# Performance work log

Hardware: AMD Instinct MI355X
Metric: run time of the kernel (lower is better)

## Reference

```python
import jax, jax.numpy as jnp
import numpy as np

INPUT_SIZE = 1024
MEMORY_SIZE = 32768
MEMORY_DIM = 128
TOP_K = 32
EPS = 1e-8


def _linear_params(key, fan_in, fan_out):
    kw, kb = jax.random.split(key)
    bound = 1.0 / np.sqrt(fan_in)
    W = jax.random.uniform(kw, (fan_out, fan_in), jnp.float32, -bound, bound)
    b = jax.random.uniform(kb, (fan_out,), jnp.float32, -bound, bound)
    return W, b


def setup_inputs() -> dict:
    key = jax.random.key(0)
    kx, km, k1, k2, k3 = jax.random.split(key, 5)
    x = jax.random.normal(kx, (16, INPUT_SIZE), jnp.float32)
    # xavier_uniform for the memory table
    xav = np.sqrt(6.0 / (MEMORY_SIZE + MEMORY_DIM))
    memory = jax.random.uniform(km, (MEMORY_SIZE, MEMORY_DIM), jnp.float32, -xav, xav)
    Ww, bw = _linear_params(k1, INPUT_SIZE, MEMORY_DIM)   # write_proj
    Wr, br = _linear_params(k2, INPUT_SIZE, MEMORY_DIM)   # read_proj
    Wo, bo = _linear_params(k3, MEMORY_DIM, INPUT_SIZE)   # output_proj
    return {"x": x, "memory": memory, "Ww": Ww, "bw": bw,
            "Wr": Wr, "br": br, "Wo": Wo, "bo": bo}


def reference(x, memory, Ww, bw, Wr, br, Wo, bo):
    # x: [B, I]; memory: [M, D] (prev_memory=None path -> shared table per batch)
    write_vector = x @ Ww.T + bw          # [B, D]
    read_query = x @ Wr.T + br            # [B, D]

    # cosine similarity of each query against every memory slot: [B, M]
    qn = jnp.maximum(jnp.linalg.norm(read_query, axis=-1, keepdims=True), EPS)  # [B, 1]
    mn = jnp.maximum(jnp.linalg.norm(memory, axis=-1), EPS)                      # [M]
    similarity = (read_query @ memory.T) / (qn * mn[None, :])

    # top-k slots; the scatter-built one-hot bmm is just a gather + sum
    _, top_idx = jax.lax.top_k(similarity, TOP_K)        # [B, k] int32
    retrieved = memory[top_idx].sum(axis=1)              # [B, D]

    output = retrieved @ Wo.T + bo                        # [B, I]

    write_strength = jax.nn.sigmoid(
        jnp.sum(write_vector * retrieved, axis=-1, keepdims=True))  # [B, 1]
    # outer-product update [B,1,D] broadcast-added over all M slots
    update = (write_strength * write_vector)[:, None, :]  # [B, 1, D]
    new_memory = memory[None, :, :] + update              # [B, M, D]
    return output, new_memory
```

## Files before the change

### kernel.cpp

```cpp
#include <hip/hip_runtime.h>
#include <math.h>

#define BATCH 16
#define ISZ   1024
#define MSZ   32768
#define DSZ   128
#define TOPK  32
#define EPSV  1e-8f
#define NCHUNK 32
#define CHUNK  (MSZ / NCHUNK)
#define CPL    (CHUNK / 64)

__global__ void proj_kernel(const float* __restrict__ x,
                            const float* __restrict__ Ww, const float* __restrict__ bw,
                            const float* __restrict__ Wr, const float* __restrict__ br,
                            float* __restrict__ wv, float* __restrict__ rq) {
    int d = blockIdx.x;
    int b = blockIdx.y;
    int lane = threadIdx.x;
    const float* xr  = x  + (size_t)b * ISZ;
    const float* wwr = Ww + (size_t)d * ISZ;
    const float* wrr = Wr + (size_t)d * ISZ;
    float aw = 0.f, ar = 0.f;
    for (int j = lane; j < ISZ; j += 64) {
        float xv = xr[j];
        aw = fmaf(xv, wwr[j], aw);
        ar = fmaf(xv, wrr[j], ar);
    }
    for (int off = 32; off; off >>= 1) {
        aw += __shfl_down(aw, off);
        ar += __shfl_down(ar, off);
    }
    if (lane == 0) {
        wv[b * DSZ + d] = aw + bw[d];
        rq[b * DSZ + d] = ar + br[d];
    }
}

__global__ __launch_bounds__(128)
void sim_kernel(const float* __restrict__ rq,
                const float* __restrict__ memory, float* __restrict__ sim) {
    __shared__ float qn_s[BATCH];
    int tid = threadIdx.x;
    {
        int b = tid >> 3, seg = tid & 7;
        float a = 0.f;
        #pragma unroll
        for (int j = 0; j < 16; ++j) {
            float v = rq[b * DSZ + seg * 16 + j];
            a = fmaf(v, v, a);
        }
        for (int off = 4; off; off >>= 1) a += __shfl_down(a, off, 8);
        if (seg == 0) qn_s[b] = fmaxf(sqrtf(a), EPSV);
    }
    __syncthreads();

    int r = blockIdx.x * 128 + tid;
    const float4* row = (const float4*)(memory + (size_t)r * DSZ);
    const float4* rq4 = (const float4*)rq;
    float acc[BATCH];
    #pragma unroll
    for (int b = 0; b < BATCH; ++b) acc[b] = 0.f;
    float nrm = 0.f;
    #pragma unroll 4
    for (int j = 0; j < 32; ++j) {
        float4 v = row[j];
        nrm = fmaf(v.x, v.x, fmaf(v.y, v.y, fmaf(v.z, v.z, fmaf(v.w, v.w, nrm))));
        #pragma unroll
        for (int b = 0; b < BATCH; ++b) {
            float4 q = rq4[b * 32 + j];
            acc[b] = fmaf(v.x, q.x, fmaf(v.y, q.y, fmaf(v.z, q.z, fmaf(v.w, q.w, acc[b]))));
        }
    }
    float mnr = fmaxf(sqrtf(nrm), EPSV);
    #pragma unroll
    for (int b = 0; b < BATCH; ++b)
        sim[(size_t)b * MSZ + r] = acc[b] / (qn_s[b] * mnr);
}

__global__ __launch_bounds__(256)
void ptopk_kernel(const float* __restrict__ sim,
                  float* __restrict__ cand_v, int* __restrict__ cand_i) {
    int lane = threadIdx.x & 63;
    int task = blockIdx.x * 4 + (threadIdx.x >> 6);
    int b     = task >> 5;
    int chunk = task & 31;
    int base  = chunk * CHUNK;
    const float* s = sim + (size_t)b * MSZ + base;

    float val[CPL];
    #pragma unroll
    for (int i = 0; i < CPL; ++i) val[i] = s[i * 64 + lane];

    float keep_v = -INFINITY; int keep_i = 0x7FFFFFFF;
    for (int k = 0; k < TOPK; ++k) {
        float lv = -INFINITY; int li = 0x7FFFFFFF;
        #pragma unroll
        for (int i = 0; i < CPL; ++i) {
            int gi = base + i * 64 + lane;
            bool better = val[i] > lv;
            lv = better ? val[i] : lv;
            li = better ? gi : li;
        }
        float bv = lv; int bi = li;
        #pragma unroll
        for (int off = 32; off; off >>= 1) {
            float ov = __shfl_xor(bv, off);
            int   oi = __shfl_xor(bi, off);
            if (ov > bv || (ov == bv && oi < bi)) { bv = ov; bi = oi; }
        }
        if (lane == k) { keep_v = bv; keep_i = bi; }
        #pragma unroll
        for (int i = 0; i < CPL; ++i) {
            int gi = base + i * 64 + lane;
            val[i] = (gi == bi) ? -INFINITY : val[i];
        }
    }
    if (lane < TOPK) {
        cand_v[task * TOPK + lane] = keep_v;
        cand_i[task * TOPK + lane] = keep_i;
    }
}

__global__ __launch_bounds__(128)
void merge_kernel(const float* __restrict__ cand_v, const int* __restrict__ cand_i,
                  const float* __restrict__ memory, const float* __restrict__ wv,
                  const float* __restrict__ Wo, const float* __restrict__ bo,
                  float* __restrict__ out, float* __restrict__ u) {
    __shared__ int   topi[TOPK];
    __shared__ float r_s[DSZ];
    __shared__ float s_sh;
    int b = blockIdx.x;
    int tid = threadIdx.x;
    int lane = tid & 63;
    const int NC = NCHUNK * TOPK;
    const int PL = NC / 64;

    if (tid < 64) {
        float val[PL]; int idx[PL];
        #pragma unroll
        for (int i = 0; i < PL; ++i) {
            val[i] = cand_v[b * NC + i * 64 + lane];
            idx[i] = cand_i[b * NC + i * 64 + lane];
        }
        for (int k = 0; k < TOPK; ++k) {
            float lv = -INFINITY; int li = 0x7FFFFFFF;
            #pragma unroll
            for (int i = 0; i < PL; ++i) {
                bool better = (val[i] > lv) || (val[i] == lv && idx[i] < li);
                lv = better ? val[i] : lv;
                li = better ? idx[i] : li;
            }
            float bv = lv; int bi = li;
            #pragma unroll
            for (int off = 32; off; off >>= 1) {
                float ov = __shfl_xor(bv, off);
                int   oi = __shfl_xor(bi, off);
                if (ov > bv || (ov == bv && oi < bi)) { bv = ov; bi = oi; }
            }
            if (lane == k) topi[lane] = bi;
            #pragma unroll
            for (int i = 0; i < PL; ++i)
                val[i] = (idx[i] == bi) ? -INFINITY : val[i];
        }
    }
    __syncthreads();

    float rsum = 0.f;
    for (int k = 0; k < TOPK; ++k)
        rsum += memory[(size_t)topi[k] * DSZ + tid];
    r_s[tid] = rsum;
    __syncthreads();

    if (tid < 64) {
        float a = wv[b * DSZ + tid] * r_s[tid] + wv[b * DSZ + 64 + tid] * r_s[64 + tid];
        for (int off = 32; off; off >>= 1) a += __shfl_down(a, off);
        if (tid == 0) s_sh = 1.f / (1.f + expf(-a));
    }
    __syncthreads();
    u[b * DSZ + tid] = s_sh * wv[b * DSZ + tid];

    const float4* r4 = (const float4*)r_s;
    for (int i = tid; i < ISZ; i += 128) {
        const float4* w4 = (const float4*)(Wo + (size_t)i * DSZ);
        float acc = 0.f;
        #pragma unroll 8
        for (int j = 0; j < 32; ++j) {
            float4 w = w4[j];
            float4 r = r4[j];
            acc = fmaf(w.x, r.x, fmaf(w.y, r.y, fmaf(w.z, r.z, fmaf(w.w, r.w, acc))));
        }
        out[b * ISZ + i] = acc + bo[i];
    }
}

__global__ void bcast_kernel(const float* __restrict__ memory, const float* __restrict__ u,
                             float* __restrict__ out_nm) {
    __shared__ float4 u_s[BATCH * DSZ / 4];
    int tid = threadIdx.x;
    const float4* u4 = (const float4*)u;
    for (int i = tid; i < BATCH * DSZ / 4; i += 256) u_s[i] = u4[i];
    __syncthreads();
    size_t f = (size_t)blockIdx.x * 256 + tid;
    float4 m4 = ((const float4*)memory)[f];
    int d4 = (int)(f & 31);
    float4* o = (float4*)out_nm;
    #pragma unroll
    for (int b = 0; b < BATCH; ++b) {
        float4 uv = u_s[b * 32 + d4];
        float4 r = make_float4(m4.x + uv.x, m4.y + uv.y, m4.z + uv.z, m4.w + uv.w);
        o[(size_t)b * (MSZ * DSZ / 4) + f] = r;
    }
}

extern "C" void kernel_launch(void* const* d_in, const int* in_sizes, int n_in,
                              void* d_out, int out_size, void* d_ws, size_t ws_size,
                              hipStream_t stream) {
    const float* x      = (const float*)d_in[0];
    const float* memory = (const float*)d_in[1];
    const float* Ww     = (const float*)d_in[2];
    const float* bw     = (const float*)d_in[3];
    const float* Wr     = (const float*)d_in[4];
    const float* br     = (const float*)d_in[5];
    const float* Wo     = (const float*)d_in[6];
    const float* bo     = (const float*)d_in[7];

    float* out    = (float*)d_out;
    float* out_nm = out + BATCH * ISZ;

    float* ws        = (float*)d_ws;
    float* wv        = ws;
    float* rq        = wv + BATCH * DSZ;
    float* sim       = rq + BATCH * DSZ;
    float* cand_v    = sim + (size_t)BATCH * MSZ;
    int*   cand_i    = (int*)(cand_v + BATCH * NCHUNK * TOPK);
    float* u         = (float*)(cand_i + BATCH * NCHUNK * TOPK);

    proj_kernel<<<dim3(DSZ, BATCH), 64, 0, stream>>>(x, Ww, bw, Wr, br, wv, rq);
    sim_kernel<<<MSZ / 128, 128, 0, stream>>>(rq, memory, sim);
    ptopk_kernel<<<(BATCH * NCHUNK) / 4, 256, 0, stream>>>(sim, cand_v, cand_i);
    merge_kernel<<<BATCH, 128, 0, stream>>>(cand_v, cand_i, memory, wv, Wo, bo, out, u);
    bcast_kernel<<<MSZ * DSZ / 4 / 256, 256, 0, stream>>>(memory, u, out_nm);
}
```

Baseline: 173.9 us.

## Fuse all five stages into one persistent kernel with grid barriers

Replaces the five separate launches (projection, similarity, partial top-k, merge, broadcast) with a single persistent kernel of 256 blocks that separates the stages with software grid-wide barriers built on atomics. Work in each stage is remapped onto the fixed grid, and the final broadcast loops over 16 tiles per block. This targets launch overhead and inter-kernel gaps, but leaves many blocks idle in the narrow stages (merge uses only 16 blocks, top-k uses half the waves). It also needs an extra memset and relies on all 256 blocks being co-resident to avoid deadlock.

```diff
diff --git a/kernel.cpp b/kernel.cpp
--- a/kernel.cpp
+++ b/kernel.cpp
@@ -10,39 +10,76 @@
 #define NCHUNK 32
 #define CHUNK  (MSZ / NCHUNK)
 #define CPL    (CHUNK / 64)
-
-__global__ void proj_kernel(const float* __restrict__ x,
-                            const float* __restrict__ Ww, const float* __restrict__ bw,
-                            const float* __restrict__ Wr, const float* __restrict__ br,
-                            float* __restrict__ wv, float* __restrict__ rq) {
-    int d = blockIdx.x;
-    int b = blockIdx.y;
-    int lane = threadIdx.x;
-    const float* xr  = x  + (size_t)b * ISZ;
-    const float* wwr = Ww + (size_t)d * ISZ;
-    const float* wrr = Wr + (size_t)d * ISZ;
-    float aw = 0.f, ar = 0.f;
-    for (int j = lane; j < ISZ; j += 64) {
-        float xv = xr[j];
-        aw = fmaf(xv, wwr[j], aw);
-        ar = fmaf(xv, wrr[j], ar);
-    }
-    for (int off = 32; off; off >>= 1) {
-        aw += __shfl_down(aw, off);
-        ar += __shfl_down(ar, off);
-    }
-    if (lane == 0) {
-        wv[b * DSZ + d] = aw + bw[d];
-        rq[b * DSZ + d] = ar + br[d];
-    }
+#define NBLOCKS  256
+#define NTHREADS 256
+
+typedef float f32x4 __attribute__((ext_vector_type(4)));
+
+__device__ __forceinline__ void grid_barrier(unsigned* bar, unsigned epoch) {
+    __syncthreads();
+    if (threadIdx.x == 0) {
+        __threadfence();
+        unsigned prev = __hip_atomic_fetch_add(&bar[0], 1u, __ATOMIC_ACQ_REL,
+                                               __HIP_MEMORY_SCOPE_AGENT);
+        if (prev == NBLOCKS - 1) {
+            __hip_atomic_store(&bar[0], 0u, __ATOMIC_RELAXED, __HIP_MEMORY_SCOPE_AGENT);
+            __hip_atomic_store(&bar[1], epoch, __ATOMIC_RELEASE, __HIP_MEMORY_SCOPE_AGENT);
+        } else {
+            while (__hip_atomic_load(&bar[1], __ATOMIC_ACQUIRE,
+                                     __HIP_MEMORY_SCOPE_AGENT) < epoch) {
+                __builtin_amdgcn_s_sleep(2);
+            }
+        }
+        __threadfence();
+    }
+    __syncthreads();
 }
 
-__global__ __launch_bounds__(128)
-void sim_kernel(const float* __restrict__ rq,
-                const float* __restrict__ memory, float* __restrict__ sim) {
+__global__ __launch_bounds__(NTHREADS)
+void fused_kernel(const float* __restrict__ x, const float* __restrict__ memory,
+                  const float* __restrict__ Ww, const float* __restrict__ bw,
+                  const float* __restrict__ Wr, const float* __restrict__ br,
+                  const float* __restrict__ Wo, const float* __restrict__ bo,
+                  float* __restrict__ wv, float* __restrict__ rq,
+                  float* __restrict__ sim, float* __restrict__ cand_v,
+                  int* __restrict__ cand_i, float* __restrict__ u,
+                  unsigned* __restrict__ bar,
+                  float* __restrict__ out, float* __restrict__ out_nm) {
     __shared__ float qn_s[BATCH];
-    int tid = threadIdx.x;
+    __shared__ int   topi[TOPK];
+    __shared__ float r_s[DSZ];
+    __shared__ float s_sh;
+    __shared__ f32x4 u_s[BATCH * DSZ / 4];
+
+    const int tid  = threadIdx.x;
+    const int bid  = blockIdx.x;
+    const int lane = tid & 63;
+    const int wid  = tid >> 6;
+
     {
+        int wg = bid * 4 + wid;
+        #pragma unroll
+        for (int t = 0; t < 4; ++t) {
+            int T   = wg * 4 + t;
+            int b   = T >> 8;
+            int d   = (T >> 1) & 127;
+            int mat = T & 1;
+            const float* wrow = (mat ? Wr : Ww) + (size_t)d * ISZ;
+            const float* xr   = x + (size_t)b * ISZ;
+            float a = 0.f;
+            #pragma unroll
+            for (int i = 0; i < 16; ++i)
+                a = fmaf(xr[lane + 64 * i], wrow[lane + 64 * i], a);
+            for (int off = 32; off; off >>= 1) a += __shfl_down(a, off);
+            if (lane == 0) {
+                if (mat) rq[b * DSZ + d] = a + br[d];
+                else     wv[b * DSZ + d] = a + bw[d];
+            }
+        }
+    }
+    grid_barrier(bar, 1);
+
+    if (tid < 128) {
         int b = tid >> 3, seg = tid & 7;
         float a = 0.f;
         #pragma unroll
@@ -54,102 +91,51 @@
         if (seg == 0) qn_s[b] = fmaxf(sqrtf(a), EPSV);
     }
     __syncthreads();
-
-    int r = blockIdx.x * 128 + tid;
-    const float4* row = (const float4*)(memory + (size_t)r * DSZ);
-    const float4* rq4 = (const float4*)rq;
-    float acc[BATCH];
-    #pragma unroll
-    for (int b = 0; b < BATCH; ++b) acc[b] = 0.f;
-    float nrm = 0.f;
-    #pragma unroll 4
-    for (int j = 0; j < 32; ++j) {
-        float4 v = row[j];
-        nrm = fmaf(v.x, v.x, fmaf(v.y, v.y, fmaf(v.z, v.z, fmaf(v.w, v.w, nrm))));
-        #pragma unroll
-        for (int b = 0; b < BATCH; ++b) {
-            float4 q = rq4[b * 32 + j];
-            acc[b] = fmaf(v.x, q.x, fmaf(v.y, q.y, fmaf(v.z, q.z, fmaf(v.w, q.w, acc[b]))));
-        }
-    }
-    float mnr = fmaxf(sqrtf(nrm), EPSV);
-    #pragma unroll
-    for (int b = 0; b < BATCH; ++b)
-        sim[(size_t)b * MSZ + r] = acc[b] / (qn_s[b] * mnr);
-}
-
-__global__ __launch_bounds__(256)
-void ptopk_kernel(const float* __restrict__ sim,
-                  float* __restrict__ cand_v, int* __restrict__ cand_i) {
-    int lane = threadIdx.x & 63;
-    int task = blockIdx.x * 4 + (threadIdx.x >> 6);
-    int b     = task >> 5;
-    int chunk = task & 31;
-    int base  = chunk * CHUNK;
-    const float* s = sim + (size_t)b * MSZ + base;
-
-    float val[CPL];
-    #pragma unroll
-    for (int i = 0; i < CPL; ++i) val[i] = s[i * 64 + lane];
-
-    float keep_v = -INFINITY; int keep_i = 0x7FFFFFFF;
-    for (int k = 0; k < TOPK; ++k) {
-        float lv = -INFINITY; int li = 0x7FFFFFFF;
-        #pragma unroll
-        for (int i = 0; i < CPL; ++i) {
-            int gi = base + i * 64 + lane;
-            bool better = val[i] > lv;
-            lv = better ? val[i] : lv;
-            li = better ? gi : li;
-        }
-        float bv = lv; int bi = li;
-        #pragma unroll
-        for (int off = 32; off; off >>= 1) {
-            float ov = __shfl_xor(bv, off);
-            int   oi = __shfl_xor(bi, off);
-            if (ov > bv || (ov == bv && oi < bi)) { bv = ov; bi = oi; }
-        }
-        if (lane == k) { keep_v = bv; keep_i = bi; }
-        #pragma unroll
-        for (int i = 0; i < CPL; ++i) {
-            int gi = base + i * 64 + lane;
-            val[i] = (gi == bi) ? -INFINITY : val[i];
-        }
-    }
-    if (lane < TOPK) {
-        cand_v[task * TOPK + lane] = keep_v;
-        cand_i[task * TOPK + lane] = keep_i;
-    }
-}
-
-__global__ __launch_bounds__(128)
-void merge_kernel(const float* __restrict__ cand_v, const int* __restrict__ cand_i,
-                  const float* __restrict__ memory, const float* __restrict__ wv,
-                  const float* __restrict__ Wo, const float* __restrict__ bo,
-                  float* __restrict__ out, float* __restrict__ u) {
-    __shared__ int   topi[TOPK];
-    __shared__ float r_s[DSZ];
-    __shared__ float s_sh;
-    int b = blockIdx.x;
-    int tid = threadIdx.x;
-    int lane = tid & 63;
-    const int NC = NCHUNK * TOPK;
-    const int PL = NC / 64;
-
-    if (tid < 64) {
-        float val[PL]; int idx[PL];
-        #pragma unroll
-        for (int i = 0; i < PL; ++i) {
-            val[i] = cand_v[b * NC + i * 64 + lane];
-            idx[i] = cand_i[b * NC + i * 64 + lane];
-        }
+    if (tid < 128) {
+        int r = bid * 128 + tid;
+        const f32x4* row = (const f32x4*)(memory + (size_t)r * DSZ);
+        const f32x4* q4  = (const f32x4*)rq;
+        float acc[BATCH];
+        #pragma unroll
+        for (int b = 0; b < BATCH; ++b) acc[b] = 0.f;
+        float nrm = 0.f;
+        #pragma unroll 4
+        for (int j = 0; j < 32; ++j) {
+            f32x4 v = row[j];
+            nrm = fmaf(v.x, v.x, fmaf(v.y, v.y, fmaf(v.z, v.z, fmaf(v.w, v.w, nrm))));
+            #pragma unroll
+            for (int b = 0; b < BATCH; ++b) {
+                f32x4 q = q4[b * 32 + j];
+                acc[b] = fmaf(v.x, q.x, fmaf(v.y, q.y, fmaf(v.z, q.z, fmaf(v.w, q.w, acc[b]))));
+            }
+        }
+        float mnr = fmaxf(sqrtf(nrm), EPSV);
+        #pragma unroll
+        for (int b = 0; b < BATCH; ++b)
+            sim[(size_t)b * MSZ + r] = acc[b] / (qn_s[b] * mnr);
+    }
+    grid_barrier(bar, 2);
+
+    if (wid < 2) {
+        int task  = bid * 2 + wid;
+        int b     = task >> 5;
+        int chunk = task & 31;
+        int base  = chunk * CHUNK;
+        const float* s = sim + (size_t)b * MSZ + base;
+
+        float val[CPL];
+        #pragma unroll
+        for (int i = 0; i < CPL; ++i) val[i] = s[i * 64 + lane];
+
+        float keep_v = -INFINITY; int keep_i = 0x7FFFFFFF;
         for (int k = 0; k < TOPK; ++k) {
             float lv = -INFINITY; int li = 0x7FFFFFFF;
             #pragma unroll
-            for (int i = 0; i < PL; ++i) {
-                bool better = (val[i] > lv) || (val[i] == lv && idx[i] < li);
+            for (int i = 0; i < CPL; ++i) {
+                int gi = base + i * 64 + lane;
+                bool better = val[i] > lv;
                 lv = better ? val[i] : lv;
-                li = better ? idx[i] : li;
+                li = better ? gi : li;
             }
             float bv = lv; int bi = li;
             #pragma unroll
@@ -158,58 +144,99 @@
                 int   oi = __shfl_xor(bi, off);
                 if (ov > bv || (ov == bv && oi < bi)) { bv = ov; bi = oi; }
             }
-            if (lane == k) topi[lane] = bi;
-            #pragma unroll
-            for (int i = 0; i < PL; ++i)
-                val[i] = (idx[i] == bi) ? -INFINITY : val[i];
-        }
-    }
-    __syncthreads();
-
-    float rsum = 0.f;
-    for (int k = 0; k < TOPK; ++k)
-        rsum += memory[(size_t)topi[k] * DSZ + tid];
-    r_s[tid] = rsum;
-    __syncthreads();
-
-    if (tid < 64) {
-        float a = wv[b * DSZ + tid] * r_s[tid] + wv[b * DSZ + 64 + tid] * r_s[64 + tid];
-        for (int off = 32; off; off >>= 1) a += __shfl_down(a, off);
-        if (tid == 0) s_sh = 1.f / (1.f + expf(-a));
-    }
-    __syncthreads();
-    u[b * DSZ + tid] = s_sh * wv[b * DSZ + tid];
-
-    const float4* r4 = (const float4*)r_s;
-    for (int i = tid; i < ISZ; i += 128) {
-        const float4* w4 = (const float4*)(Wo + (size_t)i * DSZ);
-        float acc = 0.f;
-        #pragma unroll 8
-        for (int j = 0; j < 32; ++j) {
-            float4 w = w4[j];
-            float4 r = r4[j];
-            acc = fmaf(w.x, r.x, fmaf(w.y, r.y, fmaf(w.z, r.z, fmaf(w.w, r.w, acc))));
-        }
-        out[b * ISZ + i] = acc + bo[i];
-    }
-}
-
-__global__ void bcast_kernel(const float* __restrict__ memory, const float* __restrict__ u,
-                             float* __restrict__ out_nm) {
-    __shared__ float4 u_s[BATCH * DSZ / 4];
-    int tid = threadIdx.x;
-    const float4* u4 = (const float4*)u;
-    for (int i = tid; i < BATCH * DSZ / 4; i += 256) u_s[i] = u4[i];
-    __syncthreads();
-    size_t f = (size_t)blockIdx.x * 256 + tid;
-    float4 m4 = ((const float4*)memory)[f];
-    int d4 = (int)(f & 31);
-    float4* o = (float4*)out_nm;
-    #pragma unroll
-    for (int b = 0; b < BATCH; ++b) {
-        float4 uv = u_s[b * 32 + d4];
-        float4 r = make_float4(m4.x + uv.x, m4.y + uv.y, m4.z + uv.z, m4.w + uv.w);
-        o[(size_t)b * (MSZ * DSZ / 4) + f] = r;
+            if (lane == k) { keep_v = bv; keep_i = bi; }
+            #pragma unroll
+            for (int i = 0; i < CPL; ++i) {
+                int gi = base + i * 64 + lane;
+                val[i] = (gi == bi) ? -INFINITY : val[i];
+            }
+        }
+        if (lane < TOPK) {
+            cand_v[task * TOPK + lane] = keep_v;
+            cand_i[task * TOPK + lane] = keep_i;
+        }
+    }
+    grid_barrier(bar, 3);
+
+    if (bid < BATCH) {
+        int b = bid;
+        const int NC = NCHUNK * TOPK;
+        const int PL = NC / 64;
+        if (tid < 64) {
+            float val[PL]; int idx[PL];
+            #pragma unroll
+            for (int i = 0; i < PL; ++i) {
+                val[i] = cand_v[b * NC + i * 64 + lane];
+                idx[i] = cand_i[b * NC + i * 64 + lane];
+            }
+            for (int k = 0; k < TOPK; ++k) {
+                float lv = -INFINITY; int li = 0x7FFFFFFF;
+                #pragma unroll
+                for (int i = 0; i < PL; ++i) {
+                    bool better = (val[i] > lv) || (val[i] == lv && idx[i] < li);
+                    lv = better ? val[i] : lv;
+                    li = better ? idx[i] : li;
+                }
+                float bv = lv; int bi = li;
+                #pragma unroll
+                for (int off = 32; off; off >>= 1) {
+                    float ov = __shfl_xor(bv, off);
+                    int   oi = __shfl_xor(bi, off);
+                    if (ov > bv || (ov == bv && oi < bi)) { bv = ov; bi = oi; }
+                }
+                if (lane == k) topi[lane] = bi;
+                #pragma unroll
+                for (int i = 0; i < PL; ++i)
+                    val[i] = (idx[i] == bi) ? -INFINITY : val[i];
+            }
+        }
+        __syncthreads();
+        if (tid < DSZ) {
+            float rsum = 0.f;
+            for (int k = 0; k < TOPK; ++k)
+                rsum += memory[(size_t)topi[k] * DSZ + tid];
+            r_s[tid] = rsum;
+        }
+        __syncthreads();
+        if (tid < 64) {
+            float a = wv[b * DSZ + tid] * r_s[tid] + wv[b * DSZ + 64 + tid] * r_s[64 + tid];
+            for (int off = 32; off; off >>= 1) a += __shfl_down(a, off);
+            if (tid == 0) s_sh = 1.f / (1.f + expf(-a));
+        }
+        __syncthreads();
+        if (tid < DSZ) u[b * DSZ + tid] = s_sh * wv[b * DSZ + tid];
+
+        const f32x4* r4 = (const f32x4*)r_s;
+        for (int i = tid; i < ISZ; i += NTHREADS) {
+            const f32x4* w4 = (const f32x4*)(Wo + (size_t)i * DSZ);
+            float acc = 0.f;
+            #pragma unroll 8
+            for (int j = 0; j < 32; ++j) {
+                f32x4 w = w4[j];
+                f32x4 r = r4[j];
+                acc = fmaf(w.x, r.x, fmaf(w.y, r.y, fmaf(w.z, r.z, fmaf(w.w, r.w, acc))));
+            }
+            out[b * ISZ + i] = acc + bo[i];
+        }
+    }
+    grid_barrier(bar, 4);
+
+    {
+        const f32x4* u4 = (const f32x4*)u;
+        u_s[tid]       = u4[tid];
+        u_s[tid + 256] = u4[tid + 256];
+        __syncthreads();
+        const f32x4* m = (const f32x4*)memory;
+        f32x4* o = (f32x4*)out_nm;
+        #pragma unroll 2
+        for (int it = 0; it < 16; ++it) {
+            size_t f = (size_t)bid * 4096 + (size_t)it * 256 + tid;
+            f32x4 m4 = m[f];
+            int d4 = (int)(f & 31);
+            #pragma unroll
+            for (int b = 0; b < BATCH; ++b)
+                o[(size_t)b * (MSZ * DSZ / 4) + f] = m4 + u_s[b * 32 + d4];
+        }
     }
 }
 
@@ -228,17 +255,17 @@
     float* out    = (float*)d_out;
     float* out_nm = out + BATCH * ISZ;
 
-    float* ws        = (float*)d_ws;
-    float* wv        = ws;
-    float* rq        = wv + BATCH * DSZ;
-    float* sim       = rq + BATCH * DSZ;
-    float* cand_v    = sim + (size_t)BATCH * MSZ;
-    int*   cand_i    = (int*)(cand_v + BATCH * NCHUNK * TOPK);
-    float* u         = (float*)(cand_i + BATCH * NCHUNK * TOPK);
-
-    proj_kernel<<<dim3(DSZ, BATCH), 64, 0, stream>>>(x, Ww, bw, Wr, br, wv, rq);
-    sim_kernel<<<MSZ / 128, 128, 0, stream>>>(rq, memory, sim);
-    ptopk_kernel<<<(BATCH * NCHUNK) / 4, 256, 0, stream>>>(sim, cand_v, cand_i);
-    merge_kernel<<<BATCH, 128, 0, stream>>>(cand_v, cand_i, memory, wv, Wo, bo, out, u);
-    bcast_kernel<<<MSZ * DSZ / 4 / 256, 256, 0, stream>>>(memory, u, out_nm);
+    float*    ws     = (float*)d_ws;
+    float*    wv     = ws;
+    float*    rq     = wv + BATCH * DSZ;
+    float*    sim    = rq + BATCH * DSZ;
+    float*    cand_v = sim + (size_t)BATCH * MSZ;
+    int*      cand_i = (int*)(cand_v + BATCH * NCHUNK * TOPK);
+    float*    u      = (float*)(cand_i + BATCH * NCHUNK * TOPK);
+    unsigned* bar    = (unsigned*)(u + BATCH * DSZ);
+
+    hipMemsetAsync((void*)bar, 0, 2 * sizeof(unsigned), stream);
+    fused_kernel<<<NBLOCKS, NTHREADS, 0, stream>>>(
+        x, memory, Ww, bw, Wr, br, Wo, bo,
+        wv, rq, sim, cand_v, cand_i, u, bar, out, out_nm);
 }
```

After: 305.6 us. +75.8%, slower.
